# Kernel tuning notes

Hardware: AMD Instinct MI355X
Metric: run time of the kernel (lower is better)

Reference implementation:

```python
import jax, jax.numpy as jnp
import numpy as np

N_NODES = 100000
N_EDGES = 1600000
IN_CH = 128
OUT_CH = 64
HID = 2 * OUT_CH


def setup_inputs() -> dict:
    key = jax.random.key(0)
    ks = jax.random.split(key, 9)
    x = jax.random.normal(ks[0], (N_NODES, IN_CH), dtype=jnp.float32)
    edge_index = jax.random.randint(ks[1], (2, N_EDGES), 0, N_NODES, dtype=jnp.int64)
    s = 0.05
    W1 = jax.random.normal(ks[2], (IN_CH, HID), dtype=jnp.float32) * s
    b1 = jnp.zeros((HID,), dtype=jnp.float32)
    Wmu = jax.random.normal(ks[3], (HID, OUT_CH), dtype=jnp.float32) * s
    bmu = jnp.zeros((OUT_CH,), dtype=jnp.float32)
    Wls = jax.random.normal(ks[4], (HID, OUT_CH), dtype=jnp.float32) * s
    bls = jnp.zeros((OUT_CH,), dtype=jnp.float32)
    eps = jax.random.normal(ks[5], (N_NODES, OUT_CH), dtype=jnp.float32)
    return {"x": x, "edge_index": edge_index, "W1": W1, "b1": b1,
            "Wmu": Wmu, "bmu": bmu, "Wls": Wls, "bls": bls, "eps": eps}


def _gcn_conv(x, W, b, src, dst, dis):
    # PyG GCNConv: out = D^{-1/2}(A+I)D^{-1/2} X W + b, self-loops added.
    h = x @ W  # [N, F]
    norm = dis[src] * dis[dst]  # per-edge symmetric norm
    msg = h[src] * norm[:, None]  # [E, F] gathered + scaled messages
    agg = jax.ops.segment_sum(msg, dst, num_segments=x.shape[0])
    agg = agg + h * (dis * dis)[:, None]  # self-loop term
    return agg + b


def reference(x, edge_index, W1, b1, Wmu, bmu, Wls, bls, eps):
    src, dst = edge_index[0], edge_index[1]
    N = x.shape[0]
    # degree over A + I (aggregation at dst, +1 for self loop)
    deg = jax.ops.segment_sum(jnp.ones_like(dst, dtype=x.dtype), dst,
                              num_segments=N) + 1.0
    dis = jax.lax.rsqrt(deg)  # deg >= 1, safe
    h = _gcn_conv(x, W1, b1, src, dst, dis)
    mu = _gcn_conv(h, Wmu, bmu, src, dst, dis)
    logstd = _gcn_conv(h, Wls, bls, src, dst, dis)
    z = mu + eps * jnp.exp(logstd)  # reparametrization trick
    return (z, mu, logstd)
```

## Files before the change

kernel.cpp:

```cpp
#include <hip/hip_runtime.h>
#include <hip/hip_bf16.h>


typedef unsigned int u32;
typedef unsigned short u16;
typedef __bf16 bf16x8 __attribute__((ext_vector_type(8)));
typedef float f32x4 __attribute__((ext_vector_type(4)));

__device__ __forceinline__ u16 f2bf(float f) {
    union { float f; u32 u; } v; v.f = f;
    u32 u = v.u;
    u += 0x7fffu + ((u >> 16) & 1u);
    return (u16)(u >> 16);
}
__device__ __forceinline__ float bflo(u32 p) {
    union { u32 u; float f; } v; v.u = p << 16; return v.f;
}
__device__ __forceinline__ float bfhi(u32 p) {
    union { u32 u; float f; } v; v.u = p & 0xffff0000u; return v.f;
}

__global__ __launch_bounds__(256) void deg_hist(const int* __restrict__ dst,
                                                u32* __restrict__ deg,
                                                u32* __restrict__ loc, int E) {
    int i4 = (blockIdx.x * 256 + threadIdx.x) * 4;
    if (i4 + 3 < E) {
        int4 d4 = *(const int4*)(dst + i4);
        uint4 l4;
        l4.x = atomicAdd(&deg[d4.x], 1u);
        l4.y = atomicAdd(&deg[d4.y], 1u);
        l4.z = atomicAdd(&deg[d4.z], 1u);
        l4.w = atomicAdd(&deg[d4.w], 1u);
        *(uint4*)(loc + i4) = l4;
    } else {
        for (int i = i4; i < E; ++i) loc[i] = atomicAdd(&deg[dst[i]], 1u);
    }
}

__global__ __launch_bounds__(256) void scanA(const u32* __restrict__ deg,
                                             u32* __restrict__ blockSums, int N) {
    __shared__ u32 s[256];
    int t = threadIdx.x, i = blockIdx.x * 256 + t;
    s[t] = (i < N) ? deg[i] : 0u;
    for (int off = 128; off > 0; off >>= 1) {
        __syncthreads();
        if (t < off) s[t] += s[t + off];
    }
    if (t == 0) blockSums[blockIdx.x] = s[0];
}

__global__ __launch_bounds__(512) void scanB(const u32* __restrict__ blockSums,
                                             u32* __restrict__ blockOffs, int NB) {
    __shared__ u32 s[512];
    int t = threadIdx.x;
    u32 v = (t < NB) ? blockSums[t] : 0u;
    s[t] = v;
    for (int off = 1; off < 512; off <<= 1) {
        __syncthreads();
        u32 add = (t >= off) ? s[t - off] : 0u;
        __syncthreads();
        s[t] += add;
    }
    __syncthreads();
    if (t < NB) blockOffs[t] = s[t] - v;
}

__global__ __launch_bounds__(256) void scanC(const u32* __restrict__ deg,
                                             const u32* __restrict__ blockOffs,
                                             u32* __restrict__ rowstart,
                                             float* __restrict__ dis, int N, int E) {
    __shared__ u32 s[256];
    int t = threadIdx.x, i = blockIdx.x * 256 + t;
    u32 v = (i < N) ? deg[i] : 0u;
    s[t] = v;
    for (int off = 1; off < 256; off <<= 1) {
        __syncthreads();
        u32 add = (t >= off) ? s[t - off] : 0u;
        __syncthreads();
        s[t] += add;
    }
    __syncthreads();
    if (i < N) {
        rowstart[i] = blockOffs[blockIdx.x] + s[t] - v;
        dis[i] = rsqrtf((float)v + 1.0f);
    }
    if (i == 0) rowstart[N] = (u32)E;
}

__global__ __launch_bounds__(256) void place_kernel(const int* __restrict__ src,
                                                    const int* __restrict__ dst,
                                                    const u32* __restrict__ loc,
                                                    const u32* __restrict__ rowstart,
                                                    int* __restrict__ csr, int E) {
    int i4 = (blockIdx.x * 256 + threadIdx.x) * 4;
    if (i4 + 3 < E) {
        int4 s4 = *(const int4*)(src + i4);
        int4 d4 = *(const int4*)(dst + i4);
        uint4 l4 = *(const uint4*)(loc + i4);
        csr[rowstart[d4.x] + l4.x] = s4.x;
        csr[rowstart[d4.y] + l4.y] = s4.y;
        csr[rowstart[d4.z] + l4.z] = s4.z;
        csr[rowstart[d4.w] + l4.w] = s4.w;
    } else {
        for (int i = i4; i < E; ++i) csr[rowstart[dst[i]] + loc[i]] = src[i];
    }
}

__global__ __launch_bounds__(256) void fuse_w(const float* __restrict__ W1,
                                              const float* __restrict__ Wmu,
                                              const float* __restrict__ Wls,
                                              const float* __restrict__ b1,
                                              const float* __restrict__ bmu,
                                              const float* __restrict__ bls,
                                              float* __restrict__ Wf,
                                              float* __restrict__ bb,
                                              float* __restrict__ bcat) {
    int idx = blockIdx.x * 256 + threadIdx.x;
    if (idx >= 16384) return;
    int k = idx >> 7, n = idx & 127;
    const float* Wcol = (n < 64) ? (Wmu + n) : (Wls + (n - 64));
    float acc = 0.f;
#pragma unroll 8
    for (int j = 0; j < 128; ++j) acc += W1[k * 128 + j] * Wcol[j * 64];
    Wf[idx] = acc;
    if (k == 0) {
        float accb = 0.f;
#pragma unroll 8
        for (int j = 0; j < 128; ++j) accb += b1[j] * Wcol[j * 64];
        bb[n] = accb;
        bcat[n] = (n < 64) ? bmu[n] : bls[n - 64];
    }
}

__global__ __launch_bounds__(256) void convert_x(const float* __restrict__ x,
                                                 const float* __restrict__ dis,
                                                 u32* __restrict__ xs,
                                                 u32* __restrict__ bufA, int N) {
    long i = (long)blockIdx.x * 256 + threadIdx.x;
    long node = i >> 5;
    if (node > N) return;
    if (node == N) {
        ((uint2*)xs)[i] = make_uint2(0u, 0u);
        ((uint2*)bufA)[i] = make_uint2(0u, 0u);
        return;
    }
    float dd = dis[node];
    f32x4 v = ((const f32x4*)x)[i];
    u32 p0 = (u32)f2bf(v[0] * dd) | ((u32)f2bf(v[1] * dd) << 16);
    u32 p1 = (u32)f2bf(v[2] * dd) | ((u32)f2bf(v[3] * dd) << 16);
    ((uint2*)xs)[i] = make_uint2(p0, p1);
}

__global__ __launch_bounds__(256) void gather1(const u32* __restrict__ xs,
                                               const int* __restrict__ csr,
                                               const u32* __restrict__ rowstart,
                                               const float* __restrict__ dis,
                                               u32* __restrict__ yb, int N) {
    int wid = (blockIdx.x * 256 + threadIdx.x) >> 6;
    int sub = (threadIdx.x & 63) >> 4, l = threadIdx.x & 15;
    int node = wid * 4 + sub;
    bool live = node < N;
    int nodeC = live ? node : 0;
    float dd = dis[nodeC];
    u32 beg = live ? rowstart[nodeC] : 0u;
    u32 end = live ? rowstart[nodeC + 1] : 0u;
    const uint4* xs4 = (const uint4*)xs;

    uint4 selfv = xs4[(long)nodeC * 16 + l];
    float acc0 = bflo(selfv.x), acc1 = bfhi(selfv.x);
    float acc2 = bflo(selfv.y), acc3 = bfhi(selfv.y);
    float acc4 = bflo(selfv.z), acc5 = bfhi(selfv.z);
    float acc6 = bflo(selfv.w), acc7 = bfhi(selfv.w);

    for (u32 e0 = beg; e0 < end; e0 += 16) {
        u32 cnt = min(16u, end - e0);
        int s = ((u32)l < cnt) ? csr[e0 + l] : N;
#pragma unroll 8
        for (int j = 0; j < 16; ++j) {
            int sj = __shfl(s, sub * 16 + j);
            uint4 w = xs4[(long)sj * 16 + l];
            acc0 += bflo(w.x); acc1 += bfhi(w.x);
            acc2 += bflo(w.y); acc3 += bfhi(w.y);
            acc4 += bflo(w.z); acc5 += bfhi(w.z);
            acc6 += bflo(w.w); acc7 += bfhi(w.w);
        }
    }
    if (live) {
        uint4 o;
        o.x = (u32)f2bf(acc0 * dd) | ((u32)f2bf(acc1 * dd) << 16);
        o.y = (u32)f2bf(acc2 * dd) | ((u32)f2bf(acc3 * dd) << 16);
        o.z = (u32)f2bf(acc4 * dd) | ((u32)f2bf(acc5 * dd) << 16);
        o.w = (u32)f2bf(acc6 * dd) | ((u32)f2bf(acc7 * dd) << 16);
        ((uint4*)yb)[(long)node * 16 + l] = o;
    }
}

__global__ __launch_bounds__(256) void gemm128b(const u16* A, const float* __restrict__ Bw,
                                                const float* __restrict__ bb,
                                                const float* __restrict__ dis,
                                                u16* C, int M) {
    __shared__ __align__(16) u16 Bt[128][136];
    __shared__ float bbS[128];
    int tid = threadIdx.x;
    for (int idx = tid; idx < 128 * 128; idx += 256) {
        int k = idx >> 7, n = idx & 127;
        Bt[n][k] = f2bf(Bw[idx]);
    }
    if (tid < 128) bbS[tid] = bb[tid];
    __syncthreads();

    int wave = tid >> 6, lane = tid & 63;
    int quad = lane >> 4, mn = lane & 15;
    long row0 = (long)blockIdx.x * 64 + wave * 16;
    if (row0 >= M) return;

    bf16x8 afrag[4];
    const u16* Arow = A + (row0 + mn) * 128 + quad * 8;
#pragma unroll
    for (int kk = 0; kk < 4; ++kk)
        afrag[kk] = *reinterpret_cast<const bf16x8*>(Arow + kk * 32);

    float disr[4];
#pragma unroll
    for (int r = 0; r < 4; ++r) disr[r] = dis[row0 + quad * 4 + r];

#pragma unroll
    for (int n0 = 0; n0 < 8; ++n0) {
        f32x4 acc = {0.f, 0.f, 0.f, 0.f};
#pragma unroll
        for (int kk = 0; kk < 4; ++kk) {
            bf16x8 bfrag =
                *reinterpret_cast<const bf16x8*>(&Bt[n0 * 16 + mn][kk * 32 + quad * 8]);
            acc = __builtin_amdgcn_mfma_f32_16x16x32_bf16(afrag[kk], bfrag, acc, 0, 0, 0);
        }
        int col = n0 * 16 + mn;
#pragma unroll
        for (int r = 0; r < 4; ++r)
            C[(row0 + quad * 4 + r) * 128 + col] = f2bf((acc[r] + bbS[col]) * disr[r]);
    }
}

__global__ __launch_bounds__(256) void gather2(const u32* __restrict__ ts,
                                               const int* __restrict__ csr,
                                               const u32* __restrict__ rowstart,
                                               const float* __restrict__ dis,
                                               const float* __restrict__ bcat,
                                               const float* __restrict__ eps,
                                               float* __restrict__ out, int N) {
    int wid = (blockIdx.x * 256 + threadIdx.x) >> 6;
    int sub = (threadIdx.x & 63) >> 4, l = threadIdx.x & 15;
    int node = wid * 4 + sub;
    bool live = node < N;
    int nodeC = live ? node : 0;
    float dd = dis[nodeC];
    u32 beg = live ? rowstart[nodeC] : 0u;
    u32 end = live ? rowstart[nodeC + 1] : 0u;
    const uint4* ts4 = (const uint4*)ts;

    uint4 selfv = ts4[(long)nodeC * 16 + l];
    float a0 = bflo(selfv.x), a1 = bfhi(selfv.x);
    float a2 = bflo(selfv.y), a3 = bfhi(selfv.y);
    float a4 = bflo(selfv.z), a5 = bfhi(selfv.z);
    float a6 = bflo(selfv.w), a7 = bfhi(selfv.w);

    for (u32 e0 = beg; e0 < end; e0 += 16) {
        u32 cnt = min(16u, end - e0);
        int s = ((u32)l < cnt) ? csr[e0 + l] : N;
#pragma unroll 8
        for (int j = 0; j < 16; ++j) {
            int sj = __shfl(s, sub * 16 + j);
            uint4 w = ts4[(long)sj * 16 + l];
            a0 += bflo(w.x); a1 += bfhi(w.x);
            a2 += bflo(w.y); a3 += bfhi(w.y);
            a4 += bflo(w.z); a5 += bfhi(w.z);
            a6 += bflo(w.w); a7 += bfhi(w.w);
        }
    }

    int c0 = l * 8;
    f32x4 clo = ((const f32x4*)bcat)[2 * l], chi = ((const f32x4*)bcat)[2 * l + 1];
    float v0 = a0 * dd + clo[0];
    float v1 = a1 * dd + clo[1];
    float v2 = a2 * dd + clo[2];
    float v3 = a3 * dd + clo[3];
    float v4 = a4 * dd + chi[0];
    float v5 = a5 * dd + chi[1];
    float v6 = a6 * dd + chi[2];
    float v7 = a7 * dd + chi[3];

    int srcl = (threadIdx.x & 63) + 8;
    float w0 = __shfl(v0, srcl), w1 = __shfl(v1, srcl), w2 = __shfl(v2, srcl),
          w3 = __shfl(v3, srcl), w4 = __shfl(v4, srcl), w5 = __shfl(v5, srcl),
          w6 = __shfl(v6, srcl), w7 = __shfl(v7, srcl);

    if (!live) return;
    long NO = (long)N * 64;
    if (l < 8) {
        float* mu = out + NO + (long)node * 64 + c0;
        ((f32x4*)mu)[0] = f32x4{v0, v1, v2, v3};
        ((f32x4*)mu)[1] = f32x4{v4, v5, v6, v7};
        const float* ep = eps + (long)node * 64 + c0;
        f32x4 e0v = ((const f32x4*)ep)[0], e1v = ((const f32x4*)ep)[1];
        float* z = out + (long)node * 64 + c0;
        ((f32x4*)z)[0] = f32x4{v0 + e0v[0] * __expf(w0), v1 + e0v[1] * __expf(w1),
                               v2 + e0v[2] * __expf(w2), v3 + e0v[3] * __expf(w3)};
        ((f32x4*)z)[1] = f32x4{v4 + e1v[0] * __expf(w4), v5 + e1v[1] * __expf(w5),
                               v6 + e1v[2] * __expf(w6), v7 + e1v[3] * __expf(w7)};
    } else {
        float* ls = out + 2 * NO + (long)node * 64 + (c0 - 64);
        ((f32x4*)ls)[0] = f32x4{v0, v1, v2, v3};
        ((f32x4*)ls)[1] = f32x4{v4, v5, v6, v7};
    }
}

extern "C" void kernel_launch(void* const* d_in, const int* in_sizes, int n_in,
                              void* d_out, int out_size, void* d_ws, size_t ws_size,
                              hipStream_t stream) {
    const float* x   = (const float*)d_in[0];
    const int* ei    = (const int*)d_in[1];
    const float* W1  = (const float*)d_in[2];
    const float* b1  = (const float*)d_in[3];
    const float* Wmu = (const float*)d_in[4];
    const float* bmu = (const float*)d_in[5];
    const float* Wls = (const float*)d_in[6];
    const float* bls = (const float*)d_in[7];
    const float* eps = (const float*)d_in[8];
    float* out = (float*)d_out;

    const int N = in_sizes[0] / 128;
    const int E = in_sizes[1] / 2;
    const int* src = ei;
    const int* dst = ei + E;
    const int NB = (N + 255) / 256;

    char* ws = (char*)d_ws;
    u32* deg       = (u32*)(ws + 0);
    u32* rowstart  = (u32*)(ws + 401408);
    u32* blockSums = (u32*)(ws + 802816);
    u32* blockOffs = (u32*)(ws + 804864);
    float* dis     = (float*)(ws + 806912);
    float* Wf      = (float*)(ws + 1208320);
    float* bb      = (float*)(ws + 1273856);
    float* bcat    = (float*)(ws + 1274368);
    u32* loc       = (u32*)(ws + 1274880);
    int* csr       = (int*)(ws + 7674880);
    u32* xs        = (u32*)(ws + 14074880);
    u32* bufA      = (u32*)(ws + 39675136);

    hipMemsetAsync(deg, 0, 400000, stream);

    int gridE4 = (E / 4 + 255) / 256;
    deg_hist<<<gridE4, 256, 0, stream>>>(dst, deg, loc, E);
    scanA<<<NB, 256, 0, stream>>>(deg, blockSums, N);
    scanB<<<1, 512, 0, stream>>>(blockSums, blockOffs, NB);
    scanC<<<NB, 256, 0, stream>>>(deg, blockOffs, rowstart, dis, N, E);
    place_kernel<<<gridE4, 256, 0, stream>>>(src, dst, loc, rowstart, csr, E);
    fuse_w<<<64, 256, 0, stream>>>(W1, Wmu, Wls, b1, bmu, bls, Wf, bb, bcat);

    long Qc = (long)(N + 1) * 32;
    convert_x<<<(int)((Qc + 255) / 256), 256, 0, stream>>>(x, dis, xs, bufA, N);

    int gridG = ((N + 3) / 4 * 64 + 255) / 256;
    int gemmBlocks = (N + 63) / 64;

    gather1<<<gridG, 256, 0, stream>>>(xs, csr, rowstart, dis, bufA, N);
    gemm128b<<<gemmBlocks, 256, 0, stream>>>((const u16*)bufA, Wf, bb, dis,
                                             (u16*)bufA, N);
    gather2<<<gridG, 256, 0, stream>>>(bufA, csr, rowstart, dis, bcat, eps, out, N);
}
```

Baseline: 451.5 us.

## Fuse first gather with GEMM, shrink edge slot index to u8, prefetch CSR

Merges the first neighbor aggregation and the 128x128 bf16 MFMA GEMM into one kernel. Each block aggregates 16 nodes into an LDS tile and multiplies it by a pre-transposed bf16 weight matrix read from global memory. This removes the intermediate buffer round trip and the per-block weight conversion. The per-edge slot index is stored as u8 instead of u32, which cuts histogram/placement traffic but silently breaks for any node with in-degree above 255. Both gathers now prefetch the next 16 CSR indices and batch 8 row loads before accumulating, to improve memory-level parallelism.

```diff
diff --git a/kernel.cpp b/kernel.cpp
--- a/kernel.cpp
+++ b/kernel.cpp
@@ -4,6 +4,7 @@
 
 typedef unsigned int u32;
 typedef unsigned short u16;
+typedef unsigned char u8;
 typedef __bf16 bf16x8 __attribute__((ext_vector_type(8)));
 typedef float f32x4 __attribute__((ext_vector_type(4)));
 
@@ -22,18 +23,18 @@
 
 __global__ __launch_bounds__(256) void deg_hist(const int* __restrict__ dst,
                                                 u32* __restrict__ deg,
-                                                u32* __restrict__ loc, int E) {
+                                                u8* __restrict__ loc, int E) {
     int i4 = (blockIdx.x * 256 + threadIdx.x) * 4;
     if (i4 + 3 < E) {
         int4 d4 = *(const int4*)(dst + i4);
-        uint4 l4;
-        l4.x = atomicAdd(&deg[d4.x], 1u);
-        l4.y = atomicAdd(&deg[d4.y], 1u);
-        l4.z = atomicAdd(&deg[d4.z], 1u);
-        l4.w = atomicAdd(&deg[d4.w], 1u);
-        *(uint4*)(loc + i4) = l4;
+        uchar4 l4;
+        l4.x = (u8)atomicAdd(&deg[d4.x], 1u);
+        l4.y = (u8)atomicAdd(&deg[d4.y], 1u);
+        l4.z = (u8)atomicAdd(&deg[d4.z], 1u);
+        l4.w = (u8)atomicAdd(&deg[d4.w], 1u);
+        *(uchar4*)(loc + i4) = l4;
     } else {
-        for (int i = i4; i < E; ++i) loc[i] = atomicAdd(&deg[dst[i]], 1u);
+        for (int i = i4; i < E; ++i) loc[i] = (u8)atomicAdd(&deg[dst[i]], 1u);
     }
 }
 
@@ -89,14 +90,14 @@
 
 __global__ __launch_bounds__(256) void place_kernel(const int* __restrict__ src,
                                                     const int* __restrict__ dst,
-                                                    const u32* __restrict__ loc,
+                                                    const u8* __restrict__ loc,
                                                     const u32* __restrict__ rowstart,
                                                     int* __restrict__ csr, int E) {
     int i4 = (blockIdx.x * 256 + threadIdx.x) * 4;
     if (i4 + 3 < E) {
         int4 s4 = *(const int4*)(src + i4);
         int4 d4 = *(const int4*)(dst + i4);
-        uint4 l4 = *(const uint4*)(loc + i4);
+        uchar4 l4 = *(const uchar4*)(loc + i4);
         csr[rowstart[d4.x] + l4.x] = s4.x;
         csr[rowstart[d4.y] + l4.y] = s4.y;
         csr[rowstart[d4.z] + l4.z] = s4.z;
@@ -112,7 +113,7 @@
                                               const float* __restrict__ b1,
                                               const float* __restrict__ bmu,
                                               const float* __restrict__ bls,
-                                              float* __restrict__ Wf,
+                                              u16* __restrict__ WfT,
                                               float* __restrict__ bb,
                                               float* __restrict__ bcat) {
     int idx = blockIdx.x * 256 + threadIdx.x;
@@ -122,7 +123,7 @@
     float acc = 0.f;
 #pragma unroll 8
     for (int j = 0; j < 128; ++j) acc += W1[k * 128 + j] * Wcol[j * 64];
-    Wf[idx] = acc;
+    WfT[n * 128 + k] = f2bf(acc);
     if (k == 0) {
         float accb = 0.f;
 #pragma unroll 8
@@ -135,13 +136,13 @@
 __global__ __launch_bounds__(256) void convert_x(const float* __restrict__ x,
                                                  const float* __restrict__ dis,
                                                  u32* __restrict__ xs,
-                                                 u32* __restrict__ bufA, int N) {
+                                                 u32* __restrict__ ts, int N) {
     long i = (long)blockIdx.x * 256 + threadIdx.x;
     long node = i >> 5;
     if (node > N) return;
     if (node == N) {
         ((uint2*)xs)[i] = make_uint2(0u, 0u);
-        ((uint2*)bufA)[i] = make_uint2(0u, 0u);
+        ((uint2*)ts)[i] = make_uint2(0u, 0u);
         return;
     }
     float dd = dis[node];
@@ -151,92 +152,88 @@
     ((uint2*)xs)[i] = make_uint2(p0, p1);
 }
 
-__global__ __launch_bounds__(256) void gather1(const u32* __restrict__ xs,
-                                               const int* __restrict__ csr,
-                                               const u32* __restrict__ rowstart,
-                                               const float* __restrict__ dis,
-                                               u32* __restrict__ yb, int N) {
-    int wid = (blockIdx.x * 256 + threadIdx.x) >> 6;
-    int sub = (threadIdx.x & 63) >> 4, l = threadIdx.x & 15;
-    int node = wid * 4 + sub;
+__global__ __launch_bounds__(256) void g1gemm(const u32* __restrict__ xs,
+                                              const int* __restrict__ csr,
+                                              const u32* __restrict__ rowstart,
+                                              const float* __restrict__ dis,
+                                              const u16* __restrict__ WfT,
+                                              const float* __restrict__ bb,
+                                              u16* __restrict__ ts, int N) {
+    __shared__ __align__(16) u16 ytile[16][136];
+    __shared__ float disS[16];
+    int tid = threadIdx.x, blk = blockIdx.x;
+    int wave = tid >> 6, lane = tid & 63;
+    int sub = lane >> 4, l = lane & 15;
+    int nl = wave * 4 + sub;
+    int node = blk * 16 + nl;
     bool live = node < N;
     int nodeC = live ? node : 0;
     float dd = dis[nodeC];
     u32 beg = live ? rowstart[nodeC] : 0u;
     u32 end = live ? rowstart[nodeC + 1] : 0u;
+    if (tid < 16) disS[tid] = (blk * 16 + tid < N) ? dis[blk * 16 + tid] : 0.f;
+
     const uint4* xs4 = (const uint4*)xs;
-
     uint4 selfv = xs4[(long)nodeC * 16 + l];
-    float acc0 = bflo(selfv.x), acc1 = bfhi(selfv.x);
-    float acc2 = bflo(selfv.y), acc3 = bfhi(selfv.y);
-    float acc4 = bflo(selfv.z), acc5 = bfhi(selfv.z);
-    float acc6 = bflo(selfv.w), acc7 = bfhi(selfv.w);
-
+    float a0 = bflo(selfv.x), a1 = bfhi(selfv.x);
+    float a2 = bflo(selfv.y), a3 = bfhi(selfv.y);
+    float a4 = bflo(selfv.z), a5 = bfhi(selfv.z);
+    float a6 = bflo(selfv.w), a7 = bfhi(selfv.w);
+
+    int s = (beg + (u32)l < end) ? csr[beg + l] : N;
     for (u32 e0 = beg; e0 < end; e0 += 16) {
-        u32 cnt = min(16u, end - e0);
-        int s = ((u32)l < cnt) ? csr[e0 + l] : N;
-#pragma unroll 8
-        for (int j = 0; j < 16; ++j) {
-            int sj = __shfl(s, sub * 16 + j);
-            uint4 w = xs4[(long)sj * 16 + l];
-            acc0 += bflo(w.x); acc1 += bfhi(w.x);
-            acc2 += bflo(w.y); acc3 += bfhi(w.y);
-            acc4 += bflo(w.z); acc5 += bfhi(w.z);
-            acc6 += bflo(w.w); acc7 += bfhi(w.w);
+        u32 e1 = e0 + 16;
+        int sn = (e1 < end && e1 + (u32)l < end) ? csr[e1 + l] : N;
+#pragma unroll
+        for (int h = 0; h < 2; ++h) {
+            int sj[8]; uint4 w[8];
+#pragma unroll
+            for (int j = 0; j < 8; ++j) sj[j] = __shfl(s, sub * 16 + h * 8 + j);
+#pragma unroll
+            for (int j = 0; j < 8; ++j) w[j] = xs4[(long)sj[j] * 16 + l];
+#pragma unroll
+            for (int j = 0; j < 8; ++j) {
+                a0 += bflo(w[j].x); a1 += bfhi(w[j].x);
+                a2 += bflo(w[j].y); a3 += bfhi(w[j].y);
+                a4 += bflo(w[j].z); a5 += bfhi(w[j].z);
+                a6 += bflo(w[j].w); a7 += bfhi(w[j].w);
+            }
         }
-    }
+        s = sn;
+    }
+    uint4 o = make_uint4(0u, 0u, 0u, 0u);
     if (live) {
-        uint4 o;
-        o.x = (u32)f2bf(acc0 * dd) | ((u32)f2bf(acc1 * dd) << 16);
-        o.y = (u32)f2bf(acc2 * dd) | ((u32)f2bf(acc3 * dd) << 16);
-        o.z = (u32)f2bf(acc4 * dd) | ((u32)f2bf(acc5 * dd) << 16);
-        o.w = (u32)f2bf(acc6 * dd) | ((u32)f2bf(acc7 * dd) << 16);
-        ((uint4*)yb)[(long)node * 16 + l] = o;
-    }
-}
-
-__global__ __launch_bounds__(256) void gemm128b(const u16* A, const float* __restrict__ Bw,
-                                                const float* __restrict__ bb,
-                                                const float* __restrict__ dis,
-                                                u16* C, int M) {
-    __shared__ __align__(16) u16 Bt[128][136];
-    __shared__ float bbS[128];
-    int tid = threadIdx.x;
-    for (int idx = tid; idx < 128 * 128; idx += 256) {
-        int k = idx >> 7, n = idx & 127;
-        Bt[n][k] = f2bf(Bw[idx]);
-    }
-    if (tid < 128) bbS[tid] = bb[tid];
+        o.x = (u32)f2bf(a0 * dd) | ((u32)f2bf(a1 * dd) << 16);
+        o.y = (u32)f2bf(a2 * dd) | ((u32)f2bf(a3 * dd) << 16);
+        o.z = (u32)f2bf(a4 * dd) | ((u32)f2bf(a5 * dd) << 16);
+        o.w = (u32)f2bf(a6 * dd) | ((u32)f2bf(a7 * dd) << 16);
+    }
+    *(uint4*)&ytile[nl][l * 8] = o;
     __syncthreads();
 
-    int wave = tid >> 6, lane = tid & 63;
-    int quad = lane >> 4, mn = lane & 15;
-    long row0 = (long)blockIdx.x * 64 + wave * 16;
-    if (row0 >= M) return;
-
-    bf16x8 afrag[4];
-    const u16* Arow = A + (row0 + mn) * 128 + quad * 8;
+    int quad = sub, mn = l;
+    bf16x8 af[4];
 #pragma unroll
     for (int kk = 0; kk < 4; ++kk)
-        afrag[kk] = *reinterpret_cast<const bf16x8*>(Arow + kk * 32);
-
-    float disr[4];
-#pragma unroll
-    for (int r = 0; r < 4; ++r) disr[r] = dis[row0 + quad * 4 + r];
-
-#pragma unroll
-    for (int n0 = 0; n0 < 8; ++n0) {
+        af[kk] = *reinterpret_cast<const bf16x8*>(&ytile[mn][kk * 32 + quad * 8]);
+
+#pragma unroll
+    for (int n0 = 0; n0 < 2; ++n0) {
+        int col = wave * 32 + n0 * 16 + mn;
         f32x4 acc = {0.f, 0.f, 0.f, 0.f};
 #pragma unroll
         for (int kk = 0; kk < 4; ++kk) {
-            bf16x8 bfrag =
-                *reinterpret_cast<const bf16x8*>(&Bt[n0 * 16 + mn][kk * 32 + quad * 8]);
-            acc = __builtin_amdgcn_mfma_f32_16x16x32_bf16(afrag[kk], bfrag, acc, 0, 0, 0);
+            bf16x8 bf =
+                *reinterpret_cast<const bf16x8*>(&WfT[col * 128 + kk * 32 + quad * 8]);
+            acc = __builtin_amdgcn_mfma_f32_16x16x32_bf16(af[kk], bf, acc, 0, 0, 0);
         }
-        int col = n0 * 16 + mn;
-#pragma unroll
-        for (int r = 0; r < 4; ++r)
-            C[(row0 + quad * 4 + r) * 128 + col] = f2bf((acc[r] + bbS[col]) * disr[r]);
+        float bc = bb[col];
+#pragma unroll
+        for (int r = 0; r < 4; ++r) {
+            int row = quad * 4 + r;
+            int gn = blk * 16 + row;
+            if (gn < N) ts[(long)gn * 128 + col] = f2bf((acc[r] + bc) * disS[row]);
+        }
     }
 }
 
@@ -263,18 +260,26 @@
     float a4 = bflo(selfv.z), a5 = bfhi(selfv.z);
     float a6 = bflo(selfv.w), a7 = bfhi(selfv.w);
 
+    int s = (beg + (u32)l < end) ? csr[beg + l] : N;
     for (u32 e0 = beg; e0 < end; e0 += 16) {
-        u32 cnt = min(16u, end - e0);
-        int s = ((u32)l < cnt) ? csr[e0 + l] : N;
-#pragma unroll 8
-        for (int j = 0; j < 16; ++j) {
-            int sj = __shfl(s, sub * 16 + j);
-            uint4 w = ts4[(long)sj * 16 + l];
-            a0 += bflo(w.x); a1 += bfhi(w.x);
-            a2 += bflo(w.y); a3 += bfhi(w.y);
-            a4 += bflo(w.z); a5 += bfhi(w.z);
-            a6 += bflo(w.w); a7 += bfhi(w.w);
+        u32 e1 = e0 + 16;
+        int sn = (e1 < end && e1 + (u32)l < end) ? csr[e1 + l] : N;
+#pragma unroll
+        for (int h = 0; h < 2; ++h) {
+            int sj[8]; uint4 w[8];
+#pragma unroll
+            for (int j = 0; j < 8; ++j) sj[j] = __shfl(s, sub * 16 + h * 8 + j);
+#pragma unroll
+            for (int j = 0; j < 8; ++j) w[j] = ts4[(long)sj[j] * 16 + l];
+#pragma unroll
+            for (int j = 0; j < 8; ++j) {
+                a0 += bflo(w[j].x); a1 += bfhi(w[j].x);
+                a2 += bflo(w[j].y); a3 += bfhi(w[j].y);
+                a4 += bflo(w[j].z); a5 += bfhi(w[j].z);
+                a6 += bflo(w[j].w); a7 += bfhi(w[j].w);
+            }
         }
+        s = sn;
     }
 
     int c0 = l * 8;
@@ -339,13 +344,13 @@
     u32* blockSums = (u32*)(ws + 802816);
     u32* blockOffs = (u32*)(ws + 804864);
     float* dis     = (float*)(ws + 806912);
-    float* Wf      = (float*)(ws + 1208320);
-    float* bb      = (float*)(ws + 1273856);
-    float* bcat    = (float*)(ws + 1274368);
-    u32* loc       = (u32*)(ws + 1274880);
-    int* csr       = (int*)(ws + 7674880);
-    u32* xs        = (u32*)(ws + 14074880);
-    u32* bufA      = (u32*)(ws + 39675136);
+    u16* WfT       = (u16*)(ws + 1208320);
+    float* bb      = (float*)(ws + 1241088);
+    float* bcat    = (float*)(ws + 1241600);
+    u8* loc        = (u8*)(ws + 1242112);
+    int* csr       = (int*)(ws + 2842112);
+    u32* xs        = (u32*)(ws + 9242112);
+    u32* ts        = (u32*)(ws + 34842368);
 
     hipMemsetAsync(deg, 0, 400000, stream);
 
@@ -355,16 +360,15 @@
     scanB<<<1, 512, 0, stream>>>(blockSums, blockOffs, NB);
     scanC<<<NB, 256, 0, stream>>>(deg, blockOffs, rowstart, dis, N, E);
     place_kernel<<<gridE4, 256, 0, stream>>>(src, dst, loc, rowstart, csr, E);
-    fuse_w<<<64, 256, 0, stream>>>(W1, Wmu, Wls, b1, bmu, bls, Wf, bb, bcat);
+    fuse_w<<<64, 256, 0, stream>>>(W1, Wmu, Wls, b1, bmu, bls, WfT, bb, bcat);
 
     long Qc = (long)(N + 1) * 32;
-    convert_x<<<(int)((Qc + 255) / 256), 256, 0, stream>>>(x, dis, xs, bufA, N);
+    convert_x<<<(int)((Qc + 255) / 256), 256, 0, stream>>>(x, dis, xs, ts, N);
+
+    int gridT = (N + 15) / 16;
+    g1gemm<<<gridT, 256, 0, stream>>>(xs, csr, rowstart, dis, WfT, bb,
+                                      (u16*)ts, N);
 
     int gridG = ((N + 3) / 4 * 64 + 255) / 256;
-    int gemmBlocks = (N + 63) / 64;
-
-    gather1<<<gridG, 256, 0, stream>>>(xs, csr, rowstart, dis, bufA, N);
-    gemm128b<<<gemmBlocks, 256, 0, stream>>>((const u16*)bufA, Wf, bb, dis,
-                                             (u16*)bufA, N);
-    gather2<<<gridG, 256, 0, stream>>>(bufA, csr, rowstart, dis, bcat, eps, out, N);
-}
+    gather2<<<gridG, 256, 0, stream>>>(ts, csr, rowstart, dis, bcat, eps, out, N);
+}
```

New measurement: 425.8 us. 1.06x faster.
